# Kernel tuning notes

Measured on AMD Instinct MI355X. Metric: run time of the kernel, lower is better.

Reference implementation:

```python
import jax, jax.numpy as jnp
import numpy as np

BATCH, SEQ, DIMS, HEADS = 4, 2048, 1024, 16
HEAD_DIM = DIMS // HEADS          # 64
ROT = HEAD_DIM // 2               # 32
BASE = 10000.0


def setup_inputs() -> dict:
    key = jax.random.key(0)
    k1, k2, k3, k4 = jax.random.split(key, 4)
    x = jax.random.normal(k1, (BATCH, SEQ, DIMS), jnp.float32)
    thetas = jax.random.normal(k2, (ROT,), jnp.float32) * 0.02
    theta_scale = jnp.ones((1,), jnp.float32)
    # nn.init.orthogonal_ equivalent
    a = jax.random.normal(k3, (HEAD_DIM, HEAD_DIM), jnp.float32)
    r_matrix, _ = jnp.linalg.qr(a)
    inv_freq = 1.0 / (BASE ** (jnp.arange(0, HEAD_DIM, 2, dtype=jnp.float32) / HEAD_DIM))
    # r_pairs: torch rand(rot,2)*head_dim then .long() -> ints in [0, head_dim)
    pairs = jax.random.randint(k4, (ROT, 2), 0, HEAD_DIM, dtype=jnp.int32)
    return {"x": x, "thetas": thetas, "theta_scale": theta_scale,
            "r_matrix": r_matrix, "inv_freq": inv_freq, "pairs": pairs}


def _forward(x, thetas, theta_scale, r_matrix, inv_freq, pairs):
    B, S, D = x.shape
    hd = r_matrix.shape[0]
    H = D // hd
    ts = theta_scale[0]
    xf = x.reshape(-1, hd)  # (B*S*H, hd)

    # Sequential Givens rotations: x @ G_k, applied as 2-column updates.
    # G[i,i]=c, G[j,j]=c, G[i,j]=-s, G[j,i]=s. If i==j, sequential torch
    def body(xx, k):
        i, j = pairs[k, 0], pairs[k, 1]
        th = thetas[k] * ts
        c, s = jnp.cos(th), jnp.sin(th)
        xi = xx[:, i]
        xj = xx[:, j]
        ni = xi * c + xj * s
        nj = jnp.where(i == j, xi * s, xj * c - xi * s)
        xx = xx.at[:, i].set(ni)
        xx = xx.at[:, j].set(nj)  # overwrites column i when i == j
        return xx, None

    xf, _ = jax.lax.scan(body, xf, jnp.arange(pairs.shape[0]))
    xf = xf @ r_matrix
    xh = xf.reshape(B, S, H, hd)

    # rotary sin/cos encoding (concatenated halves, not interleaved)
    pos = jnp.arange(S, dtype=x.dtype)[:, None]          # (S, 1)
    si = pos * inv_freq[None, :]                          # (S, hd//2)
    sin = jnp.sin(si)[None, :, None, :]                   # (1, S, 1, hd//2)
    cos = jnp.cos(si)[None, :, None, :]
    x1, x2 = xh[..., ::2], xh[..., 1::2]
    out = jnp.concatenate([x1 * cos - x2 * sin, x1 * sin + x2 * cos], axis=-1)
    return out.reshape(B, S, D) * jnp.sqrt(jnp.asarray(D, x.dtype))


def reference(x, thetas, theta_scale, r_matrix, inv_freq, pairs):
    return _forward(x, thetas, theta_scale, r_matrix, inv_freq, pairs)
```

## Files before the change

### kernel.cpp

```cpp
#include <hip/hip_runtime.h>
#include <math.h>

#define SEQ    2048
#define ROT    32
#define ROWS_PER_BLOCK 128
#define NTILES (131072 / ROWS_PER_BLOCK)

#define AS1 __attribute__((address_space(1)))
#define AS3 __attribute__((address_space(3)))

__global__ __launch_bounds__(256) void rotary_fused_kernel(
    const float* __restrict__ x,
    const float* __restrict__ thetas,
    const float* __restrict__ theta_scale,
    const float* __restrict__ R,
    const float* __restrict__ inv_freq,
    const int*   __restrict__ pairs,
    float*       __restrict__ out)
{
    __shared__ float Ws[64 * 64];
    __shared__ float SCc[8 * 32];
    __shared__ float SCs[8 * 32];
    __shared__ float Cs[ROT], Ss[ROT];
    __shared__ int   Pi[ROT], Pj[ROT];

    const int T    = blockIdx.x;
    const int t    = threadIdx.x;
    const int wave = t >> 6;
    const int lane = t & 63;

    #pragma unroll
    for (int i = 0; i < 4; ++i) {
        int ri  = i * 4 + wave;
        int row = ri * 4 + (lane >> 4);
        const float* gp = R + row * 64 + (lane & 15) * 4;
        __builtin_amdgcn_global_load_lds((const AS1 unsigned int*)gp,
                                         (AS3 unsigned int*)&Ws[ri * 256], 16, 0, 0);
    }

    if (t < ROT) {
        float th = thetas[t] * theta_scale[0];
        float sv, cv;
        sincosf(th, &sv, &cv);
        Cs[t] = cv; Ss[t] = sv;
        Pi[t] = pairs[2 * t]; Pj[t] = pairs[2 * t + 1];
    }

    {
        int pg = t >> 5, d = t & 31;
        int pos = (T * 8 + pg) & (SEQ - 1);
        float sv, cv;
        sincosf((float)pos * inv_freq[d], &sv, &cv);
        SCc[t] = 32.0f * cv;
        SCs[t] = 32.0f * sv;
    }

    const int rp = t >> 3;
    const int cg = t & 7;
    const int r0 = rp * 4;
    const float* xr0 = x + (size_t)T * (ROWS_PER_BLOCK * 64) + r0 * 64;
    float4 nx[4];
    #pragma unroll
    for (int m = 0; m < 4; ++m)
        nx[m] = *(const float4*)(xr0 + m * 64);

    __syncthreads();

    if (t < 64) {
        for (int k = ROT - 1; k >= 0; --k) {
            int i = Pi[k], j = Pj[k];
            float c = Cs[k], s = Ss[k];
            float wi = Ws[i * 64 + t];
            if (i != j) {
                float wj = Ws[j * 64 + t];
                Ws[i * 64 + t] = c * wi - s * wj;
                Ws[j * 64 + t] = s * wi + c * wj;
            } else {
                Ws[i * 64 + t] = s * wi;
            }
        }
    }
    __syncthreads();

    float acc[4][8];
    #pragma unroll
    for (int m = 0; m < 4; ++m)
        #pragma unroll
        for (int j = 0; j < 8; ++j) acc[m][j] = 0.0f;

    #pragma unroll 4
    for (int kk = 0; kk < 16; ++kk) {
        float4 xv[4];
        #pragma unroll
        for (int m = 0; m < 4; ++m) xv[m] = nx[m];
        if (kk < 15) {
            #pragma unroll
            for (int m = 0; m < 4; ++m)
                nx[m] = *(const float4*)(xr0 + m * 64 + ((kk + 1) << 2));
        }
        float4 wv[8];
        #pragma unroll
        for (int r = 0; r < 4; ++r) {
            wv[2 * r]     = *(const float4*)&Ws[(4 * kk + r) * 64 + cg * 8];
            wv[2 * r + 1] = *(const float4*)&Ws[(4 * kk + r) * 64 + cg * 8 + 4];
        }
        #pragma unroll
        for (int m = 0; m < 4; ++m) {
            const float xa[4] = {xv[m].x, xv[m].y, xv[m].z, xv[m].w};
            #pragma unroll
            for (int r = 0; r < 4; ++r) {
                const float4 w0 = wv[2 * r], w1 = wv[2 * r + 1];
                const float xs = xa[r];
                acc[m][0] = fmaf(xs, w0.x, acc[m][0]);
                acc[m][1] = fmaf(xs, w0.y, acc[m][1]);
                acc[m][2] = fmaf(xs, w0.z, acc[m][2]);
                acc[m][3] = fmaf(xs, w0.w, acc[m][3]);
                acc[m][4] = fmaf(xs, w1.x, acc[m][4]);
                acc[m][5] = fmaf(xs, w1.y, acc[m][5]);
                acc[m][6] = fmaf(xs, w1.z, acc[m][6]);
                acc[m][7] = fmaf(xs, w1.w, acc[m][7]);
            }
        }
    }

    const int scb = ((r0 >> 4) << 5) + cg * 4;
    const float4 cv = *(const float4*)&SCc[scb];
    const float4 sv = *(const float4*)&SCs[scb];
    const float cs4[4] = {cv.x, cv.y, cv.z, cv.w};
    const float sn4[4] = {sv.x, sv.y, sv.z, sv.w};

    float* og = out + (size_t)T * (ROWS_PER_BLOCK * 64);
    #pragma unroll
    for (int m = 0; m < 4; ++m) {
        int row = r0 + m;
        float o1[4], o2[4];
        #pragma unroll
        for (int d = 0; d < 4; ++d) {
            float a = acc[m][2 * d];
            float b = acc[m][2 * d + 1];
            o1[d] = a * cs4[d] - b * sn4[d];
            o2[d] = a * sn4[d] + b * cs4[d];
        }
        *(float4*)&og[row * 64 + cg * 4]      = make_float4(o1[0], o1[1], o1[2], o1[3]);
        *(float4*)&og[row * 64 + 32 + cg * 4] = make_float4(o2[0], o2[1], o2[2], o2[3]);
    }
}

extern "C" void kernel_launch(void* const* d_in, const int* in_sizes, int n_in,
                              void* d_out, int out_size, void* d_ws, size_t ws_size,
                              hipStream_t stream) {
    const float* x           = (const float*)d_in[0];
    const float* thetas      = (const float*)d_in[1];
    const float* theta_scale = (const float*)d_in[2];
    const float* r_matrix    = (const float*)d_in[3];
    const float* inv_freq    = (const float*)d_in[4];
    const int*   pairs       = (const int*)d_in[5];
    float*       out         = (float*)d_out;
    (void)d_ws; (void)ws_size;

    rotary_fused_kernel<<<NTILES, 256, 0, stream>>>(
        x, thetas, theta_scale, r_matrix, inv_freq, pairs, out);
}
```

Measured before the change: 106.8 us.

## Stage first half of x tile into swizzled LDS via async global-to-LDS loads

The first 32 columns of each 128-row x tile are now copied into a new XOR-swizzled LDS buffer with global_load_lds, issued before the R-matrix Givens preprocessing so the copy overlaps it. The remaining 32 columns still stream through the register prefetch path. Rows are remapped so each thread owns rows rp+32m instead of four consecutive rows, and a 4-block occupancy hint is added to launch_bounds. The aim is to hide global load latency behind the setup phase and the first half of the product. In exchange it uses extra LDS, adds a barrier, and the occupancy hint may squeeze registers.

```diff
diff --git a/kernel.cpp b/kernel.cpp
--- a/kernel.cpp
+++ b/kernel.cpp
@@ -9,7 +9,7 @@
 #define AS1 __attribute__((address_space(1)))
 #define AS3 __attribute__((address_space(3)))
 
-__global__ __launch_bounds__(256) void rotary_fused_kernel(
+__global__ __launch_bounds__(256, 4) void rotary_fused_kernel(
     const float* __restrict__ x,
     const float* __restrict__ thetas,
     const float* __restrict__ theta_scale,
@@ -19,6 +19,7 @@
     float*       __restrict__ out)
 {
     __shared__ float Ws[64 * 64];
+    __shared__ float Xs[128 * 8 * 4];
     __shared__ float SCc[8 * 32];
     __shared__ float SCs[8 * 32];
     __shared__ float Cs[ROT], Ss[ROT];
@@ -45,6 +46,29 @@
         Cs[t] = cv; Ss[t] = sv;
         Pi[t] = pairs[2 * t]; Pj[t] = pairs[2 * t + 1];
     }
+    __syncthreads();
+
+    const float* xg = x + (size_t)T * (ROWS_PER_BLOCK * 64);
+
+    #pragma unroll
+    for (int i = 0; i < 4; ++i) {
+        int s   = i * 256 + t;
+        int row = s >> 3;
+        int kkl = s & 7;
+        const float* gp = xg + row * 64 + ((kkl ^ (row & 7)) << 2);
+        __builtin_amdgcn_global_load_lds((const AS1 unsigned int*)gp,
+                                         (AS3 unsigned int*)&Xs[(i * 256 + wave * 64) * 4],
+                                         16, 0, 0);
+    }
+
+    const int rp   = t >> 3;
+    const int cg   = t & 7;
+    const int xoff = rp & 7;
+
+    float4 nx[4];
+    #pragma unroll
+    for (int m = 0; m < 4; ++m)
+        nx[m] = *(const float4*)(xg + (rp + 32 * m) * 64 + 32);
 
     {
         int pg = t >> 5, d = t & 31;
@@ -54,17 +78,6 @@
         SCc[t] = 32.0f * cv;
         SCs[t] = 32.0f * sv;
     }
-
-    const int rp = t >> 3;
-    const int cg = t & 7;
-    const int r0 = rp * 4;
-    const float* xr0 = x + (size_t)T * (ROWS_PER_BLOCK * 64) + r0 * 64;
-    float4 nx[4];
-    #pragma unroll
-    for (int m = 0; m < 4; ++m)
-        nx[m] = *(const float4*)(xr0 + m * 64);
-
-    __syncthreads();
 
     if (t < 64) {
         for (int k = ROT - 1; k >= 0; --k) {
@@ -89,15 +102,7 @@
         for (int j = 0; j < 8; ++j) acc[m][j] = 0.0f;
 
     #pragma unroll 4
-    for (int kk = 0; kk < 16; ++kk) {
-        float4 xv[4];
-        #pragma unroll
-        for (int m = 0; m < 4; ++m) xv[m] = nx[m];
-        if (kk < 15) {
-            #pragma unroll
-            for (int m = 0; m < 4; ++m)
-                nx[m] = *(const float4*)(xr0 + m * 64 + ((kk + 1) << 2));
-        }
+    for (int kk = 0; kk < 8; ++kk) {
         float4 wv[8];
         #pragma unroll
         for (int r = 0; r < 4; ++r) {
@@ -106,7 +111,9 @@
         }
         #pragma unroll
         for (int m = 0; m < 4; ++m) {
-            const float xa[4] = {xv[m].x, xv[m].y, xv[m].z, xv[m].w};
+            const float4 xv = *(const float4*)
+                &Xs[(((rp + 32 * m) << 3) + (kk ^ xoff)) << 2];
+            const float xa[4] = {xv.x, xv.y, xv.z, xv.w};
             #pragma unroll
             for (int r = 0; r < 4; ++r) {
                 const float4 w0 = wv[2 * r], w1 = wv[2 * r + 1];
@@ -123,16 +130,50 @@
         }
     }
 
-    const int scb = ((r0 >> 4) << 5) + cg * 4;
-    const float4 cv = *(const float4*)&SCc[scb];
-    const float4 sv = *(const float4*)&SCs[scb];
-    const float cs4[4] = {cv.x, cv.y, cv.z, cv.w};
-    const float sn4[4] = {sv.x, sv.y, sv.z, sv.w};
+    #pragma unroll 4
+    for (int kk = 8; kk < 16; ++kk) {
+        float4 xv4[4];
+        #pragma unroll
+        for (int m = 0; m < 4; ++m) xv4[m] = nx[m];
+        if (kk < 15) {
+            #pragma unroll
+            for (int m = 0; m < 4; ++m)
+                nx[m] = *(const float4*)(xg + (rp + 32 * m) * 64 + ((kk + 1) << 2));
+        }
+        float4 wv[8];
+        #pragma unroll
+        for (int r = 0; r < 4; ++r) {
+            wv[2 * r]     = *(const float4*)&Ws[(4 * kk + r) * 64 + cg * 8];
+            wv[2 * r + 1] = *(const float4*)&Ws[(4 * kk + r) * 64 + cg * 8 + 4];
+        }
+        #pragma unroll
+        for (int m = 0; m < 4; ++m) {
+            const float xa[4] = {xv4[m].x, xv4[m].y, xv4[m].z, xv4[m].w};
+            #pragma unroll
+            for (int r = 0; r < 4; ++r) {
+                const float4 w0 = wv[2 * r], w1 = wv[2 * r + 1];
+                const float xs = xa[r];
+                acc[m][0] = fmaf(xs, w0.x, acc[m][0]);
+                acc[m][1] = fmaf(xs, w0.y, acc[m][1]);
+                acc[m][2] = fmaf(xs, w0.z, acc[m][2]);
+                acc[m][3] = fmaf(xs, w0.w, acc[m][3]);
+                acc[m][4] = fmaf(xs, w1.x, acc[m][4]);
+                acc[m][5] = fmaf(xs, w1.y, acc[m][5]);
+                acc[m][6] = fmaf(xs, w1.z, acc[m][6]);
+                acc[m][7] = fmaf(xs, w1.w, acc[m][7]);
+            }
+        }
+    }
 
     float* og = out + (size_t)T * (ROWS_PER_BLOCK * 64);
     #pragma unroll
     for (int m = 0; m < 4; ++m) {
-        int row = r0 + m;
+        const int row = rp + 32 * m;
+        const int scb = ((row >> 4) << 5) + cg * 4;
+        const float4 cv = *(const float4*)&SCc[scb];
+        const float4 sv = *(const float4*)&SCs[scb];
+        const float cs4[4] = {cv.x, cv.y, cv.z, cv.w};
+        const float sn4[4] = {sv.x, sv.y, sv.z, sv.w};
         float o1[4], o2[4];
         #pragma unroll
         for (int d = 0; d < 4; ++d) {
```

Result: slower. 154.7 us (+44.9%).
